# Kernel optimization log

Hardware: AMD Instinct MI355X
Metric: run time of the kernel (lower is better)

The kernel has to match this reference:

```python
import jax, jax.numpy as jnp
import numpy as np

B, L, D, T = 32, 512, 1024, 256
MAX_MENTION_LEN = 10
NEG_INF = float('-inf')


def _static_bounds_and_keep():
    # Full (start, end) grid, flattened row-major like torch's .view(-1, 2)
    s = np.repeat(np.arange(L), L)
    e = np.tile(np.arange(L), L)
    bounds = np.stack([s, e], axis=-1)            # [L*L, 2]
    keep = (e - s) <= MAX_MENTION_LEN             # static per-position mask
    idx = np.nonzero(keep)[0]
    return jnp.asarray(bounds[keep], jnp.int32), jnp.asarray(idx, jnp.int32)


def setup_inputs() -> dict:
    key = jax.random.key(0)
    k0, k1, k2 = jax.random.split(key, 3)
    text_encodings = jax.random.normal(k0, (B, L, D), dtype=jnp.float32)
    mask_ctxt = jnp.ones((B, L), dtype=jnp.int32)
    # word -> wordpiece mapping: [start, end_exclusive); values kept in [1, L)
    tokens_mapping = jax.random.randint(k1, (B, T, 2), 1, L).astype(jnp.int32)
    W = jax.random.normal(k2, (D, 3), dtype=jnp.float32) * 0.02
    b = jnp.zeros((3,), dtype=jnp.float32)
    return {"text_encodings": text_encodings, "mask_ctxt": mask_ctxt,
            "tokens_mapping": tokens_mapping, "W": W, "b": b}


def reference(text_encodings, mask_ctxt, tokens_mapping, W, b):
    # per-token start / end / mention logits
    logits = jnp.einsum('bld,dk->blk', text_encodings, W) + b  # [B, L, 3]
    valid_tok = (mask_ctxt == 1)
    start_lp = jnp.where(valid_tok, logits[:, :, 0], NEG_INF)
    end_lp = jnp.where(valid_tok, logits[:, :, 1], NEG_INF)
    mention_lp = jnp.where(valid_tok, logits[:, :, 2], NEG_INF)

    # scores[b, s, e] = start[b, s] + end[b, e] + sum_{i=s..e} mention[b, i]
    scores = start_lp[:, :, None] + end_lp[:, None, :]          # [B, L, L]
    csum = jnp.cumsum(mention_lp, axis=1)                        # [B, L]
    csum_prev = jnp.concatenate(
        [jnp.zeros((csum.shape[0], 1), csum.dtype), csum[:, :-1]], axis=1)
    scores = scores + (csum[:, None, :] - csum_prev[:, :, None])

    # mention_sizes > 0  <=>  e >= s
    pos = jnp.arange(L)
    size_ok = pos[None, :, None] <= pos[None, None, :]           # [1, L, L]

    # token-boundary masks (scatter 1 at word starts / ends, zero col 0)
    bidx = jnp.arange(tokens_mapping.shape[0])[:, None]
    ts = jnp.zeros(mask_ctxt.shape, jnp.int32).at[bidx, tokens_mapping[:, :, 0]].set(1)
    ts = ts.at[:, 0].set(0)
    te = jnp.zeros(mask_ctxt.shape, jnp.int32).at[bidx, tokens_mapping[:, :, 1] - 1].set(1)
    te = te.at[:, 0].set(0)
    vse = ts[:, :, None] * te[:, None, :]                        # bmm outer product

    valid = size_ok & (mask_ctxt[:, :, None] > 0) & (vse > 0)
    scores = jnp.where(valid, scores, NEG_INF)

    scores_flat = scores.reshape(scores.shape[0], -1)            # [B, L*L]
    bounds_keep, keep_idx = _static_bounds_and_keep()
    out_scores = scores_flat[:, keep_idx]                        # [B, K]
    out_bounds = jnp.broadcast_to(bounds_keep[None],
                                  (scores.shape[0],) + bounds_keep.shape)
    return out_scores, out_bounds
```

## Files before the change

### kernel.cpp

```cpp
#include <hip/hip_runtime.h>
#include <math.h>

#define BB 32
#define LL 512
#define DD 1024
#define TT 256
#define NK 136393
#define NK_LIN 131273
#define S_LIN 502
#define NEG_BIG  -3.0e38f
#define NEG_MASK -1.0e30f
#define P_TOT (BB * NK)
#define FILL_THREADS (P_TOT / 4)
#define FILL_BLOCKS ((FILL_THREADS + 255) / 256)
#define GEMV_BLOCKS (BB * LL / 4)

typedef float f4v __attribute__((ext_vector_type(4)));

__device__ __forceinline__ int off_s(int s) {
    return (s <= S_LIN) ? s * (s + 21) / 2 : NK_LIN + (s - S_LIN) * LL;
}

__global__ __launch_bounds__(256) void mega_kernel(
    const float* __restrict__ text, const float* __restrict__ W,
    const float* __restrict__ bias, const int* __restrict__ mask,
    float* __restrict__ out,
    float* __restrict__ slp, float* __restrict__ elp, float* __restrict__ mlp)
{
    if (blockIdx.x < FILL_BLOCKS) {
        const int i = blockIdx.x * 256 + threadIdx.x;
        if (i >= FILL_THREADS) return;
        const int idx = i * 4;

        f4v neg = {NEG_BIG, NEG_BIG, NEG_BIG, NEG_BIG};
        *(f4v*)(out + idx) = neg;

        int k = idx - (idx / NK) * NK;
        int s, e;
        if (k >= NK_LIN) {
            const int r = k - NK_LIN;
            s = S_LIN + (r >> 9);
            e = r & 511;
        } else {
            float f = sqrtf(8.0f * (float)k + 441.0f);
            s = (int)((f - 21.0f) * 0.5f);
            if (s < 0) s = 0;
            if (s > 501) s = 501;
            while ((s + 1) * (s + 22) / 2 <= k) ++s;
            while (s * (s + 21) / 2 > k) --s;
            e = k - s * (s + 21) / 2;
        }
        float bs[8];
#pragma unroll
        for (int j = 0; j < 4; ++j) {
            bs[2 * j] = (float)s; bs[2 * j + 1] = (float)e;
            ++e;
            const int rowlen = (s <= S_LIN) ? (s + 11) : LL;
            if (e >= rowlen) { e = 0; if (++s >= LL) s = 0; }
        }
        f4v* bp = (f4v*)(out + (size_t)P_TOT + (size_t)2 * idx);
        f4v b0 = {bs[0], bs[1], bs[2], bs[3]};
        f4v b1 = {bs[4], bs[5], bs[6], bs[7]};
        bp[0] = b0; bp[1] = b1;
        return;
    }

    const int gb   = blockIdx.x - FILL_BLOCKS;
    const int wid  = threadIdx.x >> 6;
    const int lane = threadIdx.x & 63;
    const int row  = gb * 4 + wid;

    const f4v* t4 = (const f4v*)(text + (size_t)row * DD);
    const f4v* w4 = (const f4v*)W;
    float a0 = 0.f, a1 = 0.f, a2 = 0.f;
#pragma unroll
    for (int j = 0; j < 4; ++j) {
        const int fi = lane + j * 64;
        f4v v  = t4[fi];
        f4v w0 = w4[fi * 3 + 0];
        f4v w1 = w4[fi * 3 + 1];
        f4v w2 = w4[fi * 3 + 2];
        a0 += v.x * w0.x;  a1 += v.x * w0.y;  a2 += v.x * w0.z;
        a0 += v.y * w0.w;  a1 += v.y * w1.x;  a2 += v.y * w1.y;
        a0 += v.z * w1.z;  a1 += v.z * w1.w;  a2 += v.z * w2.x;
        a0 += v.w * w2.y;  a1 += v.w * w2.z;  a2 += v.w * w2.w;
    }
#pragma unroll
    for (int o = 32; o; o >>= 1) {
        a0 += __shfl_down(a0, o);
        a1 += __shfl_down(a1, o);
        a2 += __shfl_down(a2, o);
    }
    if (lane == 0) {
        const int m = mask[row];
        slp[row] = (m == 1) ? a0 + bias[0] : NEG_MASK;
        elp[row] = (m == 1) ? a1 + bias[1] : NEG_MASK;
        mlp[row] = (m == 1) ? a2 + bias[2] : NEG_MASK;
    }
}

__global__ __launch_bounds__(512) void scatter_kernel(
    const float* __restrict__ slp, const float* __restrict__ elp,
    const float* __restrict__ mlp, const int* __restrict__ mask,
    const int* __restrict__ tmap, float* __restrict__ out)
{
    const int b = blockIdx.x;
    const int t = threadIdx.x;
    __shared__ float sl[LL], el[LL], ml[LL];
    __shared__ unsigned char tsl[LL], tel[LL];

    tsl[t] = 0; tel[t] = 0;
    const int idx = b * LL + t;
    sl[t] = slp[idx]; el[t] = elp[idx]; ml[t] = mlp[idx];
    __syncthreads();
    if (t < TT) {
        int s0 = tmap[((size_t)b * TT + t) * 2 + 0];
        int e0 = tmap[((size_t)b * TT + t) * 2 + 1] - 1;
        s0 = min(max(s0, 0), LL - 1);
        e0 = min(max(e0, 0), LL - 1);
        tsl[s0] = 1;
        tel[e0] = 1;
    }
    __syncthreads();

    const int s = t;
    if (s > 0 && tsl[s] && mask[idx] == 1) {
        const size_t obase = (size_t)b * NK + off_s(s);
        const float sv = sl[s];
        const int emax = min(LL - 1, s + 10);
        float w = 0.f;
        for (int e = s; e <= emax; ++e) {
            w += ml[e];
            if (tel[e]) {
                float sc = sv + el[e] + w;
                if (sc < -1.0e29f) sc = NEG_BIG;
                out[obase + e] = sc;
            }
        }
    }
}

extern "C" void kernel_launch(void* const* d_in, const int* in_sizes, int n_in,
                              void* d_out, int out_size, void* d_ws, size_t ws_size,
                              hipStream_t stream) {
    const float* text = (const float*)d_in[0];
    const int*   mask = (const int*)d_in[1];
    const int*   tmap = (const int*)d_in[2];
    const float* W    = (const float*)d_in[3];
    const float* bias = (const float*)d_in[4];
    float* out = (float*)d_out;

    float* slp = (float*)d_ws;
    float* elp = slp + (size_t)BB * LL;
    float* mlp = elp + (size_t)BB * LL;

    mega_kernel<<<FILL_BLOCKS + GEMV_BLOCKS, 256, 0, stream>>>(
        text, W, bias, mask, out, slp, elp, mlp);
    scatter_kernel<<<BB, 512, 0, stream>>>(slp, elp, mlp, mask, tmap, out);
}
```

Before: 29.22 us.

## Fuse fill and scatter into single output-driven emit kernel after GEMV

Splits the GEMV into its own kernel and replaces the separate NEG fill plus per-batch scatter pass with one emit kernel. Each thread computes its four output scores directly from the logits and the token-boundary masks. This removes the double write of the scores region and the poorly parallel 32-block scatter. In exchange every emit block rebuilds boundary masks for up to two batches from tmap, and each valid entry sums mention logits with a short loop read from global memory.

```diff
diff --git a/kernel.cpp b/kernel.cpp
--- a/kernel.cpp
+++ b/kernel.cpp
@@ -13,65 +13,20 @@
 #define P_TOT (BB * NK)
 #define FILL_THREADS (P_TOT / 4)
 #define FILL_BLOCKS ((FILL_THREADS + 255) / 256)
-#define GEMV_BLOCKS (BB * LL / 4)
 
 typedef float f4v __attribute__((ext_vector_type(4)));
 
-__device__ __forceinline__ int off_s(int s) {
-    return (s <= S_LIN) ? s * (s + 21) / 2 : NK_LIN + (s - S_LIN) * LL;
-}
-
-__global__ __launch_bounds__(256) void mega_kernel(
+__global__ __launch_bounds__(256) void gemv_kernel(
     const float* __restrict__ text, const float* __restrict__ W,
     const float* __restrict__ bias, const int* __restrict__ mask,
-    float* __restrict__ out,
     float* __restrict__ slp, float* __restrict__ elp, float* __restrict__ mlp)
 {
-    if (blockIdx.x < FILL_BLOCKS) {
-        const int i = blockIdx.x * 256 + threadIdx.x;
-        if (i >= FILL_THREADS) return;
-        const int idx = i * 4;
-
-        f4v neg = {NEG_BIG, NEG_BIG, NEG_BIG, NEG_BIG};
-        *(f4v*)(out + idx) = neg;
-
-        int k = idx - (idx / NK) * NK;
-        int s, e;
-        if (k >= NK_LIN) {
-            const int r = k - NK_LIN;
-            s = S_LIN + (r >> 9);
-            e = r & 511;
-        } else {
-            float f = sqrtf(8.0f * (float)k + 441.0f);
-            s = (int)((f - 21.0f) * 0.5f);
-            if (s < 0) s = 0;
-            if (s > 501) s = 501;
-            while ((s + 1) * (s + 22) / 2 <= k) ++s;
-            while (s * (s + 21) / 2 > k) --s;
-            e = k - s * (s + 21) / 2;
-        }
-        float bs[8];
-#pragma unroll
-        for (int j = 0; j < 4; ++j) {
-            bs[2 * j] = (float)s; bs[2 * j + 1] = (float)e;
-            ++e;
-            const int rowlen = (s <= S_LIN) ? (s + 11) : LL;
-            if (e >= rowlen) { e = 0; if (++s >= LL) s = 0; }
-        }
-        f4v* bp = (f4v*)(out + (size_t)P_TOT + (size_t)2 * idx);
-        f4v b0 = {bs[0], bs[1], bs[2], bs[3]};
-        f4v b1 = {bs[4], bs[5], bs[6], bs[7]};
-        bp[0] = b0; bp[1] = b1;
-        return;
-    }
-
-    const int gb   = blockIdx.x - FILL_BLOCKS;
     const int wid  = threadIdx.x >> 6;
     const int lane = threadIdx.x & 63;
-    const int row  = gb * 4 + wid;
-
+    const int row  = blockIdx.x * 4 + wid;
     const f4v* t4 = (const f4v*)(text + (size_t)row * DD);
     const f4v* w4 = (const f4v*)W;
+
     float a0 = 0.f, a1 = 0.f, a2 = 0.f;
 #pragma unroll
     for (int j = 0; j < 4; ++j) {
@@ -99,45 +54,79 @@
     }
 }
 
-__global__ __launch_bounds__(512) void scatter_kernel(
+__global__ __launch_bounds__(256) void emit_kernel(
     const float* __restrict__ slp, const float* __restrict__ elp,
     const float* __restrict__ mlp, const int* __restrict__ mask,
     const int* __restrict__ tmap, float* __restrict__ out)
 {
-    const int b = blockIdx.x;
+    __shared__ unsigned char ts0[LL], te0[LL], ts1[LL], te1[LL];
     const int t = threadIdx.x;
-    __shared__ float sl[LL], el[LL], ml[LL];
-    __shared__ unsigned char tsl[LL], tel[LL];
+    const int i = blockIdx.x * 256 + t;
+    const int idx0 = blockIdx.x * 1024;
+    const int b0 = idx0 / NK;
+    const int bX = min(b0 + 1, BB - 1);
 
-    tsl[t] = 0; tel[t] = 0;
-    const int idx = b * LL + t;
-    sl[t] = slp[idx]; el[t] = elp[idx]; ml[t] = mlp[idx];
+    ts0[t] = 0; ts0[t + 256] = 0; te0[t] = 0; te0[t + 256] = 0;
+    ts1[t] = 0; ts1[t + 256] = 0; te1[t] = 0; te1[t + 256] = 0;
     __syncthreads();
-    if (t < TT) {
-        int s0 = tmap[((size_t)b * TT + t) * 2 + 0];
-        int e0 = tmap[((size_t)b * TT + t) * 2 + 1] - 1;
-        s0 = min(max(s0, 0), LL - 1);
-        e0 = min(max(e0, 0), LL - 1);
-        tsl[s0] = 1;
-        tel[e0] = 1;
+    {
+        int s0 = tmap[((size_t)b0 * TT + t) * 2 + 0];
+        int e0 = tmap[((size_t)b0 * TT + t) * 2 + 1] - 1;
+        s0 = min(max(s0, 0), LL - 1); e0 = min(max(e0, 0), LL - 1);
+        ts0[s0] = 1; te0[e0] = 1;
+        int s1 = tmap[((size_t)bX * TT + t) * 2 + 0];
+        int e1 = tmap[((size_t)bX * TT + t) * 2 + 1] - 1;
+        s1 = min(max(s1, 0), LL - 1); e1 = min(max(e1, 0), LL - 1);
+        ts1[s1] = 1; te1[e1] = 1;
     }
     __syncthreads();
 
-    const int s = t;
-    if (s > 0 && tsl[s] && mask[idx] == 1) {
-        const size_t obase = (size_t)b * NK + off_s(s);
-        const float sv = sl[s];
-        const int emax = min(LL - 1, s + 10);
-        float w = 0.f;
-        for (int e = s; e <= emax; ++e) {
-            w += ml[e];
-            if (tel[e]) {
-                float sc = sv + el[e] + w;
-                if (sc < -1.0e29f) sc = NEG_BIG;
-                out[obase + e] = sc;
-            }
+    if (i >= FILL_THREADS) return;
+    const int idx = i * 4;
+
+    int b = idx / NK;
+    int k = idx - b * NK;
+    int s, e;
+    if (k >= NK_LIN) {
+        const int r = k - NK_LIN;
+        s = S_LIN + (r >> 9);
+        e = r & 511;
+    } else {
+        float f = sqrtf(8.0f * (float)k + 441.0f);
+        s = (int)((f - 21.0f) * 0.5f);
+        if (s < 0) s = 0;
+        if (s > 501) s = 501;
+        while ((s + 1) * (s + 22) / 2 <= k) ++s;
+        while (s * (s + 21) / 2 > k) --s;
+        e = k - s * (s + 21) / 2;
+    }
+
+    float sc[4], bnd[8];
+#pragma unroll
+    for (int j = 0; j < 4; ++j) {
+        float v = NEG_BIG;
+        const unsigned char* ts = (b == b0) ? ts0 : ts1;
+        const unsigned char* te = (b == b0) ? te0 : te1;
+        if (s > 0 && e >= s && ts[s] && te[e] && mask[b * LL + s] == 1) {
+            const int base = b * LL;
+            float w = 0.f;
+            for (int l = s; l <= e; ++l) w += mlp[base + l];
+            v = slp[base + s] + elp[base + e] + w;
+            if (v < -1.0e29f) v = NEG_BIG;
         }
+        sc[j] = v;
+        bnd[2 * j] = (float)s; bnd[2 * j + 1] = (float)e;
+        ++e;
+        const int rowlen = (s <= S_LIN) ? (s + 11) : LL;
+        if (e >= rowlen) { e = 0; if (++s >= LL) { s = 0; ++b; } }
     }
+
+    f4v sv = {sc[0], sc[1], sc[2], sc[3]};
+    *(f4v*)(out + idx) = sv;
+    f4v* bp = (f4v*)(out + (size_t)P_TOT + (size_t)2 * idx);
+    f4v bv0 = {bnd[0], bnd[1], bnd[2], bnd[3]};
+    f4v bv1 = {bnd[4], bnd[5], bnd[6], bnd[7]};
+    bp[0] = bv0; bp[1] = bv1;
 }
 
 extern "C" void kernel_launch(void* const* d_in, const int* in_sizes, int n_in,
@@ -154,7 +143,7 @@
     float* elp = slp + (size_t)BB * LL;
     float* mlp = elp + (size_t)BB * LL;
 
-    mega_kernel<<<FILL_BLOCKS + GEMV_BLOCKS, 256, 0, stream>>>(
-        text, W, bias, mask, out, slp, elp, mlp);
-    scatter_kernel<<<BB, 512, 0, stream>>>(slp, elp, mlp, mask, tmap, out);
+    gemv_kernel<<<BB * LL / 4, 256, 0, stream>>>(text, W, bias, mask,
+                                                 slp, elp, mlp);
+    emit_kernel<<<FILL_BLOCKS, 256, 0, stream>>>(slp, elp, mlp, mask, tmap, out);
 }
```

After: 33.03 us. 13.0% more time.

## Restructure fill to per-row blocks, interleave GEMV blocks, tail writes full row segments

Applied to the files above, without the earlier changes.

The fill work is reorganised so that each block handles one (batch, start) row. It writes NEG_BIG only for the pre-diagonal prefix, using aligned vector nontemporal stores, and writes the bounds pairs directly without the sqrt-based index inversion. GEMV blocks are interleaved one in five with the fill blocks so the memory-bound and compute phases overlap across CUs. The tail kernel now writes every diagonal-band entry (score or NEG_BIG), reading logits from global memory instead of shared. This avoids double-writing the band region and removes the per-element index decode, but the tail kernel now stores serially from only 32 blocks and uses strided per-thread writes.

```diff
diff --git a/kernel.cpp b/kernel.cpp
--- a/kernel.cpp
+++ b/kernel.cpp
@@ -11,11 +11,12 @@
 #define NEG_BIG  -3.0e38f
 #define NEG_MASK -1.0e30f
 #define P_TOT (BB * NK)
-#define FILL_THREADS (P_TOT / 4)
-#define FILL_BLOCKS ((FILL_THREADS + 255) / 256)
-#define GEMV_BLOCKS (BB * LL / 4)
+#define GEMV_BLOCKS 4096
+#define FILL_BLOCKS 16384
+#define MEGA_BLOCKS 20480
 
 typedef float f4v __attribute__((ext_vector_type(4)));
+typedef float f2v __attribute__((ext_vector_type(2)));
 
 __device__ __forceinline__ int off_s(int s) {
     return (s <= S_LIN) ? s * (s + 21) / 2 : NK_LIN + (s - S_LIN) * LL;
@@ -27,91 +28,84 @@
     float* __restrict__ out,
     float* __restrict__ slp, float* __restrict__ elp, float* __restrict__ mlp)
 {
-    if (blockIdx.x < FILL_BLOCKS) {
-        const int i = blockIdx.x * 256 + threadIdx.x;
-        if (i >= FILL_THREADS) return;
-        const int idx = i * 4;
-
-        f4v neg = {NEG_BIG, NEG_BIG, NEG_BIG, NEG_BIG};
-        *(f4v*)(out + idx) = neg;
-
-        int k = idx - (idx / NK) * NK;
-        int s, e;
-        if (k >= NK_LIN) {
-            const int r = k - NK_LIN;
-            s = S_LIN + (r >> 9);
-            e = r & 511;
-        } else {
-            float f = sqrtf(8.0f * (float)k + 441.0f);
-            s = (int)((f - 21.0f) * 0.5f);
-            if (s < 0) s = 0;
-            if (s > 501) s = 501;
-            while ((s + 1) * (s + 22) / 2 <= k) ++s;
-            while (s * (s + 21) / 2 > k) --s;
-            e = k - s * (s + 21) / 2;
-        }
-        float bs[8];
+    const int id = blockIdx.x;
+    const int q5 = id / 5;
+    if (id - q5 * 5 == 0) {
+        const int wid  = threadIdx.x >> 6;
+        const int lane = threadIdx.x & 63;
+        const int row  = q5 * 4 + wid;
+        const f4v* t4 = (const f4v*)(text + (size_t)row * DD);
+        const f4v* w4 = (const f4v*)W;
+        float a0 = 0.f, a1 = 0.f, a2 = 0.f;
 #pragma unroll
         for (int j = 0; j < 4; ++j) {
-            bs[2 * j] = (float)s; bs[2 * j + 1] = (float)e;
-            ++e;
-            const int rowlen = (s <= S_LIN) ? (s + 11) : LL;
-            if (e >= rowlen) { e = 0; if (++s >= LL) s = 0; }
+            const int fi = lane + j * 64;
+            f4v v  = t4[fi];
+            f4v w0 = w4[fi * 3 + 0];
+            f4v w1 = w4[fi * 3 + 1];
+            f4v w2 = w4[fi * 3 + 2];
+            a0 += v.x * w0.x;  a1 += v.x * w0.y;  a2 += v.x * w0.z;
+            a0 += v.y * w0.w;  a1 += v.y * w1.x;  a2 += v.y * w1.y;
+            a0 += v.z * w1.z;  a1 += v.z * w1.w;  a2 += v.z * w2.x;
+            a0 += v.w * w2.y;  a1 += v.w * w2.z;  a2 += v.w * w2.w;
         }
-        f4v* bp = (f4v*)(out + (size_t)P_TOT + (size_t)2 * idx);
-        f4v b0 = {bs[0], bs[1], bs[2], bs[3]};
-        f4v b1 = {bs[4], bs[5], bs[6], bs[7]};
-        bp[0] = b0; bp[1] = b1;
+#pragma unroll
+        for (int o = 32; o; o >>= 1) {
+            a0 += __shfl_down(a0, o);
+            a1 += __shfl_down(a1, o);
+            a2 += __shfl_down(a2, o);
+        }
+        if (lane == 0) {
+            const int m = mask[row];
+            slp[row] = (m == 1) ? a0 + bias[0] : NEG_MASK;
+            elp[row] = (m == 1) ? a1 + bias[1] : NEG_MASK;
+            mlp[row] = (m == 1) ? a2 + bias[2] : NEG_MASK;
+        }
         return;
     }
 
-    const int gb   = blockIdx.x - FILL_BLOCKS;
-    const int wid  = threadIdx.x >> 6;
-    const int lane = threadIdx.x & 63;
-    const int row  = gb * 4 + wid;
+    const int fid = id - q5 - 1;
+    const int b = fid >> 9;
+    const int s = fid & 511;
+    const int rowlen = (s <= S_LIN) ? (s + 11) : LL;
+    const int flat0 = b * NK + off_s(s);
+    const int t = threadIdx.x;
+    const float sf = (float)s;
 
-    const f4v* t4 = (const f4v*)(text + (size_t)row * DD);
-    const f4v* w4 = (const f4v*)W;
-    float a0 = 0.f, a1 = 0.f, a2 = 0.f;
-#pragma unroll
-    for (int j = 0; j < 4; ++j) {
-        const int fi = lane + j * 64;
-        f4v v  = t4[fi];
-        f4v w0 = w4[fi * 3 + 0];
-        f4v w1 = w4[fi * 3 + 1];
-        f4v w2 = w4[fi * 3 + 2];
-        a0 += v.x * w0.x;  a1 += v.x * w0.y;  a2 += v.x * w0.z;
-        a0 += v.y * w0.w;  a1 += v.y * w1.x;  a2 += v.y * w1.y;
-        a0 += v.z * w1.z;  a1 += v.z * w1.w;  a2 += v.z * w2.x;
-        a0 += v.w * w2.y;  a1 += v.w * w2.z;  a2 += v.w * w2.w;
+    const int a = (4 - (flat0 & 3)) & 3;
+    const int head = min(s, a);
+    const int nb = (s - head) >> 2;
+    const int rem = (s - head) & 3;
+    if (t < nb) {
+        f4v neg = {NEG_BIG, NEG_BIG, NEG_BIG, NEG_BIG};
+        __builtin_nontemporal_store(neg, (f4v*)(out + flat0 + head + 4 * t));
+    } else if (t >= 248 && t < 248 + head) {
+        __builtin_nontemporal_store(NEG_BIG, out + flat0 + (t - 248));
+    } else if (t >= 252 && t < 252 + rem) {
+        __builtin_nontemporal_store(NEG_BIG, out + flat0 + head + 4 * nb + (t - 252));
     }
-#pragma unroll
-    for (int o = 32; o; o >>= 1) {
-        a0 += __shfl_down(a0, o);
-        a1 += __shfl_down(a1, o);
-        a2 += __shfl_down(a2, o);
+
+    f2v* bp = (f2v*)(out + (size_t)P_TOT);
+    if (t < rowlen) {
+        f2v v = {sf, (float)t};
+        __builtin_nontemporal_store(v, &bp[flat0 + t]);
     }
-    if (lane == 0) {
-        const int m = mask[row];
-        slp[row] = (m == 1) ? a0 + bias[0] : NEG_MASK;
-        elp[row] = (m == 1) ? a1 + bias[1] : NEG_MASK;
-        mlp[row] = (m == 1) ? a2 + bias[2] : NEG_MASK;
+    const int t2 = t + 256;
+    if (t2 < rowlen) {
+        f2v v = {sf, (float)t2};
+        __builtin_nontemporal_store(v, &bp[flat0 + t2]);
     }
 }
 
-__global__ __launch_bounds__(512) void scatter_kernel(
+__global__ __launch_bounds__(512) void tail_kernel(
     const float* __restrict__ slp, const float* __restrict__ elp,
     const float* __restrict__ mlp, const int* __restrict__ mask,
     const int* __restrict__ tmap, float* __restrict__ out)
 {
     const int b = blockIdx.x;
     const int t = threadIdx.x;
-    __shared__ float sl[LL], el[LL], ml[LL];
     __shared__ unsigned char tsl[LL], tel[LL];
-
     tsl[t] = 0; tel[t] = 0;
-    const int idx = b * LL + t;
-    sl[t] = slp[idx]; el[t] = elp[idx]; ml[t] = mlp[idx];
     __syncthreads();
     if (t < TT) {
         int s0 = tmap[((size_t)b * TT + t) * 2 + 0];
@@ -124,19 +118,22 @@
     __syncthreads();
 
     const int s = t;
-    if (s > 0 && tsl[s] && mask[idx] == 1) {
-        const size_t obase = (size_t)b * NK + off_s(s);
-        const float sv = sl[s];
-        const int emax = min(LL - 1, s + 10);
-        float w = 0.f;
-        for (int e = s; e <= emax; ++e) {
-            w += ml[e];
+    const int base = b * LL;
+    const int rowlen = (s <= S_LIN) ? (s + 11) : LL;
+    const int flat0 = b * NK + off_s(s);
+    const bool fss = (s > 0) && tsl[s] && (mask[base + s] == 1);
+    const float sv = fss ? slp[base + s] : 0.f;
+    float w = 0.f;
+    for (int e = s; e < rowlen; ++e) {
+        float v = NEG_BIG;
+        if (fss) {
+            w += mlp[base + e];
             if (tel[e]) {
-                float sc = sv + el[e] + w;
-                if (sc < -1.0e29f) sc = NEG_BIG;
-                out[obase + e] = sc;
+                v = sv + elp[base + e] + w;
+                if (v < -1.0e29f) v = NEG_BIG;
             }
         }
+        out[flat0 + e] = v;
     }
 }
 
@@ -154,7 +151,7 @@
     float* elp = slp + (size_t)BB * LL;
     float* mlp = elp + (size_t)BB * LL;
 
-    mega_kernel<<<FILL_BLOCKS + GEMV_BLOCKS, 256, 0, stream>>>(
-        text, W, bias, mask, out, slp, elp, mlp);
-    scatter_kernel<<<BB, 512, 0, stream>>>(slp, elp, mlp, mask, tmap, out);
+    mega_kernel<<<MEGA_BLOCKS, 256, 0, stream>>>(text, W, bias, mask, out,
+                                                 slp, elp, mlp);
+    tail_kernel<<<BB, 512, 0, stream>>>(slp, elp, mlp, mask, tmap, out);
 }
```

Result: slower. 33.69 us (+15.3%).

## Interleave GEMV, memset and bounds blocks in mega kernel with period-9 schedule

Applied to the files above, without the earlier changes.

Block IDs are remapped so that each group of nine blocks holds four GEMV blocks, four score-memset blocks and one bounds block. This mixes the compute-heavy and store-heavy work across the grid instead of running all fill blocks before the GEMV blocks. Bounds are now computed once per position and written for 16 batches per thread, which removes the repeated integer-sqrt index math. The cost is a more complex block decode, some idle blocks at the tail of each role, and strided scattered f2v stores for the bounds.

```diff
diff --git a/kernel.cpp b/kernel.cpp
--- a/kernel.cpp
+++ b/kernel.cpp
@@ -11,11 +11,18 @@
 #define NEG_BIG  -3.0e38f
 #define NEG_MASK -1.0e30f
 #define P_TOT (BB * NK)
-#define FILL_THREADS (P_TOT / 4)
-#define FILL_BLOCKS ((FILL_THREADS + 255) / 256)
-#define GEMV_BLOCKS (BB * LL / 4)
+#define SC4 (P_TOT / 4)
+#define GEMV_BLOCKS 4096
+#define MEMSET_BLOCKS ((SC4 + 255) / 256)
+#define BCHUNKS ((NK + 255) / 256)
+#define BGROUPS 2
+#define BOUNDS_BLOCKS (BCHUNKS * BGROUPS)
+#define PERIOD 9
+#define QMAX 1066
+#define MEGA_BLOCKS (PERIOD * QMAX)
 
 typedef float f4v __attribute__((ext_vector_type(4)));
+typedef float f2v __attribute__((ext_vector_type(2)));
 
 __device__ __forceinline__ int off_s(int s) {
     return (s <= S_LIN) ? s * (s + 21) / 2 : NK_LIN + (s - S_LIN) * LL;
@@ -27,75 +34,82 @@
     float* __restrict__ out,
     float* __restrict__ slp, float* __restrict__ elp, float* __restrict__ mlp)
 {
-    if (blockIdx.x < FILL_BLOCKS) {
-        const int i = blockIdx.x * 256 + threadIdx.x;
-        if (i >= FILL_THREADS) return;
-        const int idx = i * 4;
+    const int id = blockIdx.x;
+    const int q  = id / PERIOD;
+    const int r  = id - q * PERIOD;
 
-        f4v neg = {NEG_BIG, NEG_BIG, NEG_BIG, NEG_BIG};
-        *(f4v*)(out + idx) = neg;
-
-        int k = idx - (idx / NK) * NK;
-        int s, e;
-        if (k >= NK_LIN) {
-            const int r = k - NK_LIN;
-            s = S_LIN + (r >> 9);
-            e = r & 511;
-        } else {
-            float f = sqrtf(8.0f * (float)k + 441.0f);
-            s = (int)((f - 21.0f) * 0.5f);
-            if (s < 0) s = 0;
-            if (s > 501) s = 501;
-            while ((s + 1) * (s + 22) / 2 <= k) ++s;
-            while (s * (s + 21) / 2 > k) --s;
-            e = k - s * (s + 21) / 2;
-        }
-        float bs[8];
+    if (r < 4) {
+        const int g = q * 4 + r;
+        if (g >= GEMV_BLOCKS) return;
+        const int wid  = threadIdx.x >> 6;
+        const int lane = threadIdx.x & 63;
+        const int row  = g * 4 + wid;
+        const f4v* t4 = (const f4v*)(text + (size_t)row * DD);
+        const f4v* w4 = (const f4v*)W;
+        float a0 = 0.f, a1 = 0.f, a2 = 0.f;
 #pragma unroll
         for (int j = 0; j < 4; ++j) {
-            bs[2 * j] = (float)s; bs[2 * j + 1] = (float)e;
-            ++e;
-            const int rowlen = (s <= S_LIN) ? (s + 11) : LL;
-            if (e >= rowlen) { e = 0; if (++s >= LL) s = 0; }
+            const int fi = lane + j * 64;
+            f4v v  = t4[fi];
+            f4v w0 = w4[fi * 3 + 0];
+            f4v w1 = w4[fi * 3 + 1];
+            f4v w2 = w4[fi * 3 + 2];
+            a0 += v.x * w0.x;  a1 += v.x * w0.y;  a2 += v.x * w0.z;
+            a0 += v.y * w0.w;  a1 += v.y * w1.x;  a2 += v.y * w1.y;
+            a0 += v.z * w1.z;  a1 += v.z * w1.w;  a2 += v.z * w2.x;
+            a0 += v.w * w2.y;  a1 += v.w * w2.z;  a2 += v.w * w2.w;
         }
-        f4v* bp = (f4v*)(out + (size_t)P_TOT + (size_t)2 * idx);
-        f4v b0 = {bs[0], bs[1], bs[2], bs[3]};
-        f4v b1 = {bs[4], bs[5], bs[6], bs[7]};
-        bp[0] = b0; bp[1] = b1;
+#pragma unroll
+        for (int o = 32; o; o >>= 1) {
+            a0 += __shfl_down(a0, o);
+            a1 += __shfl_down(a1, o);
+            a2 += __shfl_down(a2, o);
+        }
+        if (lane == 0) {
+            const int m = mask[row];
+            slp[row] = (m == 1) ? a0 + bias[0] : NEG_MASK;
+            elp[row] = (m == 1) ? a1 + bias[1] : NEG_MASK;
+            mlp[row] = (m == 1) ? a2 + bias[2] : NEG_MASK;
+        }
         return;
     }
 
-    const int gb   = blockIdx.x - FILL_BLOCKS;
-    const int wid  = threadIdx.x >> 6;
-    const int lane = threadIdx.x & 63;
-    const int row  = gb * 4 + wid;
+    if (r < 8) {
+        const int m = q * 4 + (r - 4);
+        if (m >= MEMSET_BLOCKS) return;
+        const int i = m * 256 + threadIdx.x;
+        if (i < SC4) {
+            f4v neg = {NEG_BIG, NEG_BIG, NEG_BIG, NEG_BIG};
+            ((f4v*)out)[i] = neg;
+        }
+        return;
+    }
 
-    const f4v* t4 = (const f4v*)(text + (size_t)row * DD);
-    const f4v* w4 = (const f4v*)W;
-    float a0 = 0.f, a1 = 0.f, a2 = 0.f;
+    if (q >= BOUNDS_BLOCKS) return;
+    const int c = q % BCHUNKS;
+    const int g = q / BCHUNKS;
+    const int p = c * 256 + threadIdx.x;
+    if (p >= NK) return;
+    int s, e;
+    if (p >= NK_LIN) {
+        const int rr = p - NK_LIN;
+        s = S_LIN + (rr >> 9);
+        e = rr & 511;
+    } else {
+        float f = sqrtf(8.0f * (float)p + 441.0f);
+        s = (int)((f - 21.0f) * 0.5f);
+        if (s < 0) s = 0;
+        if (s > 501) s = 501;
+        while ((s + 1) * (s + 22) / 2 <= p) ++s;
+        while (s * (s + 21) / 2 > p) --s;
+        e = p - s * (s + 21) / 2;
+    }
+    f2v v = {(float)s, (float)e};
+    f2v* bp = (f2v*)(out + (size_t)P_TOT);
 #pragma unroll
-    for (int j = 0; j < 4; ++j) {
-        const int fi = lane + j * 64;
-        f4v v  = t4[fi];
-        f4v w0 = w4[fi * 3 + 0];
-        f4v w1 = w4[fi * 3 + 1];
-        f4v w2 = w4[fi * 3 + 2];
-        a0 += v.x * w0.x;  a1 += v.x * w0.y;  a2 += v.x * w0.z;
-        a0 += v.y * w0.w;  a1 += v.y * w1.x;  a2 += v.y * w1.y;
-        a0 += v.z * w1.z;  a1 += v.z * w1.w;  a2 += v.z * w2.x;
-        a0 += v.w * w2.y;  a1 += v.w * w2.z;  a2 += v.w * w2.w;
-    }
-#pragma unroll
-    for (int o = 32; o; o >>= 1) {
-        a0 += __shfl_down(a0, o);
-        a1 += __shfl_down(a1, o);
-        a2 += __shfl_down(a2, o);
-    }
-    if (lane == 0) {
-        const int m = mask[row];
-        slp[row] = (m == 1) ? a0 + bias[0] : NEG_MASK;
-        elp[row] = (m == 1) ? a1 + bias[1] : NEG_MASK;
-        mlp[row] = (m == 1) ? a2 + bias[2] : NEG_MASK;
+    for (int j = 0; j < 16; ++j) {
+        const int b = g * 16 + j;
+        bp[(size_t)b * NK + p] = v;
     }
 }
 
@@ -154,7 +168,7 @@
     float* elp = slp + (size_t)BB * LL;
     float* mlp = elp + (size_t)BB * LL;
 
-    mega_kernel<<<FILL_BLOCKS + GEMV_BLOCKS, 256, 0, stream>>>(
-        text, W, bias, mask, out, slp, elp, mlp);
+    mega_kernel<<<MEGA_BLOCKS, 256, 0, stream>>>(text, W, bias, mask, out,
+                                                 slp, elp, mlp);
     scatter_kernel<<<BB, 512, 0, stream>>>(slp, elp, mlp, mask, tmap, out);
 }
```

Measured after the change: 28.53 us. 1.02x faster.
